# Kernel optimization log

Measured on AMD Instinct MI355X. Metric: run time of the kernel, lower is better.

## Reference

```python
import jax, jax.numpy as jnp
import numpy as np

B, L, D, H = 2, 2048, 1024, 16
DK = D // H  # 64


def setup_inputs() -> dict:
    key = jax.random.key(0)
    ks = jax.random.split(key, 9)
    s = 0.02
    return {
        "x": jax.random.normal(ks[0], (B, L, D), dtype=jnp.float32),
        "wq": jax.random.normal(ks[1], (D, D), dtype=jnp.float32) * s,
        "bq": jax.random.normal(ks[2], (D,), dtype=jnp.float32) * s,
        "wk": jax.random.normal(ks[3], (D, D), dtype=jnp.float32) * s,
        "bk": jax.random.normal(ks[4], (D,), dtype=jnp.float32) * s,
        "wv": jax.random.normal(ks[5], (D, D), dtype=jnp.float32) * s,
        "bv": jax.random.normal(ks[6], (D,), dtype=jnp.float32) * s,
        "wo": jax.random.normal(ks[7], (D, D), dtype=jnp.float32) * s,
        "bo": jax.random.normal(ks[8], (D,), dtype=jnp.float32) * s,
    }


def reference(x, wq, bq, wk, bk, wv, bv, wo, bo):
    b, l, d = x.shape
    # torch nn.Linear: y = x @ W^T + b
    q = (x @ wq.T + bq).reshape(b, l, H, DK).transpose(0, 2, 1, 3)  # (b,h,l,dk)
    k = (x @ wk.T + bk).reshape(b, l, H, DK).transpose(0, 2, 1, 3)
    v = (x @ wv.T + bv).reshape(b, l, H, DK).transpose(0, 2, 1, 3)
    scale = 1.0 / jnp.sqrt(jnp.asarray(DK, dtype=x.dtype))
    scores = jnp.einsum("bhqd,bhkd->bhqk", q, k) * scale  # (b,h,l,l)
    causal = jnp.triu(jnp.ones((l, l), dtype=bool), k=1)  # True above diagonal -> masked
    scores = jnp.where(causal[None, None], -jnp.inf, scores)
    probs = jax.nn.softmax(scores, axis=-1)
    out = jnp.einsum("bhqk,bhkd->bhqd", probs, v)  # (b,h,l,dk)
    out = out.transpose(0, 2, 1, 3).reshape(b, l, d)
    return out @ wo.T + bo
```

## Files before the change

### kernel.cpp

```cpp
#include <hip/hip_runtime.h>
#include <cstdint>

#define SEQ     2048
#define DMODEL  1024
#define NHEAD   16
#define DKH     64
#define NTOK    4096
#define LDQKV   3072

typedef __bf16 bf16x8 __attribute__((ext_vector_type(8)));
typedef __bf16 bf16x4 __attribute__((ext_vector_type(4)));
typedef float  f32x4  __attribute__((ext_vector_type(4)));

#define MFMA_BF16(a, b, c) __builtin_amdgcn_mfma_f32_16x16x32_bf16((a), (b), (c), 0, 0, 0)

#define C2F 0.18033688f

__device__ inline float fast_exp2(float x) {
#if __has_builtin(__builtin_amdgcn_exp2f)
  return __builtin_amdgcn_exp2f(x);
#else
  return __expf(x * 0.69314718056f);
#endif
}

__device__ inline void async_copy16(const void* g, void* l) {
  __builtin_amdgcn_global_load_lds(
      reinterpret_cast<const __attribute__((address_space(1))) void*>(
          reinterpret_cast<uintptr_t>(g)),
      reinterpret_cast<__attribute__((address_space(3))) void*>(
          reinterpret_cast<uintptr_t>(l)),
      16, 0, 0);
}

__device__ inline bf16x4 cvt4(float4 v) {
  bf16x4 r;
  r[0] = (__bf16)v.x; r[1] = (__bf16)v.y; r[2] = (__bf16)v.z; r[3] = (__bf16)v.w;
  return r;
}

__global__ __launch_bounds__(256) void pack_kernel(
    const float4* __restrict__ x,
    const float4* __restrict__ wq, const float4* __restrict__ wk,
    const float4* __restrict__ wv, const float4* __restrict__ wo,
    const float4* __restrict__ bq, const float4* __restrict__ bk,
    const float4* __restrict__ bv,
    bf16x4* __restrict__ xb, bf16x4* __restrict__ wqkv,
    bf16x4* __restrict__ wob, float4* __restrict__ bcat)
{
  const int NX = NTOK * DMODEL / 4;
  const int NW = DMODEL * DMODEL / 4;
  const int TOT = NX + 4 * NW + 3 * (DMODEL / 4);
  for (int g = blockIdx.x * 256 + threadIdx.x; g < TOT; g += gridDim.x * 256) {
    if (g < NX) {
      xb[g] = cvt4(x[g]);
    } else if (g < NX + 3 * NW) {
      int g2 = g - NX;
      const float4* s = (g2 < NW) ? wq : (g2 < 2 * NW ? wk : wv);
      float4 v = s[g2 & (NW - 1)];
      if (g2 < NW) { v.x *= C2F; v.y *= C2F; v.z *= C2F; v.w *= C2F; }
      wqkv[g2] = cvt4(v);
    } else if (g < NX + 4 * NW) {
      int g3 = g - NX - 3 * NW;
      wob[g3] = cvt4(wo[g3]);
    } else {
      int g4 = g - NX - 4 * NW;
      const float4* s = (g4 < 256) ? bq : (g4 < 512 ? bk : bv);
      float4 v = s[g4 & 255];
      if (g4 < 256) { v.x *= C2F; v.y *= C2F; v.z *= C2F; v.w *= C2F; }
      bcat[g4] = v;
    }
  }
}

template<int BN>
__global__ __launch_bounds__(256) void gemm_bias(
    const __bf16* __restrict__ A, const __bf16* __restrict__ W,
    const float* __restrict__ bias, void* __restrict__ C,
    int ldc, int out_bf16)
{
  constexpr int K = 1024;
  constexpr int JT = BN / 32;
  __shared__ __bf16 sA[2][128 * 32];
  __shared__ __bf16 sB[2][BN * 32];
  const int tid  = threadIdx.x;
  const int wave = tid >> 6, lane = tid & 63;
  const int quad = lane >> 4, l16 = lane & 15;
  const size_t m0 = (size_t)blockIdx.x * 128;
  const size_t n0 = (size_t)blockIdx.y * BN;
  const int wm = (wave & 1) * 64, wn = (wave >> 1) * (BN / 2);

  const int g0 = wave * 2;
  const int sr = lane >> 2;
  const int sc = (lane & 3) * 8;
  const __bf16* pa0 = A + (m0 + g0 * 16 + sr) * K + sc;
  const __bf16* pa1 = pa0 + 16 * K;
  const int brow = (BN == 128) ? g0 * 16 : wave * 16;
  const __bf16* pb0 = W + (n0 + brow + sr) * K + sc;
  const int lo  = g0 * 512;
  const int lob = (BN == 128) ? g0 * 512 : wave * 512;

  f32x4 acc[4][JT];
  const f32x4 z = {0.f, 0.f, 0.f, 0.f};
#pragma unroll
  for (int i = 0; i < 4; ++i)
#pragma unroll
    for (int j = 0; j < JT; ++j) acc[i][j] = z;

  async_copy16(pa0, &sA[0][lo]);
  async_copy16(pa1, &sA[0][lo + 512]);
  async_copy16(pb0, &sB[0][lob]);
  if (BN == 128) async_copy16(pb0 + 16 * K, &sB[0][lob + 512]);

  for (int k0 = 0; k0 < K; k0 += 32) {
    const int cur = (k0 >> 5) & 1, nxt = cur ^ 1;
    __syncthreads();
    if (k0 + 32 < K) {
      async_copy16(pa0 + k0 + 32, &sA[nxt][lo]);
      async_copy16(pa1 + k0 + 32, &sA[nxt][lo + 512]);
      async_copy16(pb0 + k0 + 32, &sB[nxt][lob]);
      if (BN == 128) async_copy16(pb0 + 16 * K + k0 + 32, &sB[nxt][lob + 512]);
    }

    bf16x8 af[4], bw[JT];
#pragma unroll
    for (int i = 0; i < 4; ++i)
      af[i] = *(const bf16x8*)(&sA[cur][(wm + i * 16 + l16) * 32 + quad * 8]);
#pragma unroll
    for (int j = 0; j < JT; ++j)
      bw[j] = *(const bf16x8*)(&sB[cur][(wn + j * 16 + l16) * 32 + quad * 8]);
#pragma unroll
    for (int i = 0; i < 4; ++i)
#pragma unroll
      for (int j = 0; j < JT; ++j)
        acc[i][j] = MFMA_BF16(af[i], bw[j], acc[i][j]);
  }

  float bi[JT];
#pragma unroll
  for (int j = 0; j < JT; ++j) bi[j] = bias[n0 + wn + j * 16 + l16];

#pragma unroll
  for (int i = 0; i < 4; ++i) {
#pragma unroll
    for (int j = 0; j < JT; ++j) {
#pragma unroll
      for (int r = 0; r < 4; ++r) {
        size_t row = m0 + wm + i * 16 + quad * 4 + r;
        size_t col = n0 + wn + j * 16 + l16;
        float v = acc[i][j][r] + bi[j];
        if (out_bf16) ((__bf16*)C)[row * ldc + col] = (__bf16)v;
        else          ((float*)C)[row * ldc + col] = v;
      }
    }
  }
}

__global__ __launch_bounds__(256) void vtrans_kernel(
    const __bf16* __restrict__ qkv, __bf16* __restrict__ vt)
{
  __shared__ __bf16 t[64][66];
  const int tid = threadIdx.x;
  const int bh = blockIdx.x;
  const int b = bh >> 4, h = bh & 15;
  const int l0 = blockIdx.y * 64;
  const int r4 = tid >> 6;
  const int c  = tid & 63;
#pragma unroll
  for (int rep = 0; rep < 16; ++rep) {
    int ll = rep * 4 + r4;
    t[ll][c] = qkv[(size_t)(b * SEQ + l0 + ll) * LDQKV + 2048 + h * DKH + c];
  }
  __syncthreads();
#pragma unroll
  for (int rep = 0; rep < 16; ++rep) {
    int dk = rep * 4 + r4;
    vt[(size_t)(bh * DKH + dk) * SEQ + l0 + c] = t[c][dk];
  }
}

__global__ __launch_bounds__(256) void attn_kernel(
    const __bf16* __restrict__ qkv,
    const __bf16* __restrict__ vt,
    __bf16* __restrict__ attn)
{
  __shared__ __bf16 sK[2][64 * 64];
  __shared__ __bf16 sV[2][64 * 64];
  __shared__ __bf16 pbuf[4][16 * 64];
  const int tid  = threadIdx.x;
  const int wave = tid >> 6, lane = tid & 63;
  const int quad = lane >> 4, l16 = lane & 15;
  const int id = blockIdx.x;
  const int u = (id >> 3) & 31, v = id & 7, w = id >> 8;
  const int bh = v * 4 + w;
  const int ue = u ^ ((w >> 1) << 3);
  const int qb = (w & 1) ? ue : 31 - ue;
  const int b = bh >> 4, h = bh & 15;
  const int q0 = qb * 64;
  const int qw = q0 + wave * 16;
  const size_t tokbase = (size_t)b * SEQ;

  const int srow = lane >> 3;
  const int sgr  = (lane & 7) ^ srow;
  const __bf16* pKsrc = qkv + (tokbase + wave * 16 + srow) * LDQKV + 1024 + h * DKH + sgr * 8;
  const __bf16* pVsrc = vt + ((size_t)bh * DKH + wave * 16 + srow) * SEQ + sgr * 8;
  const int lo = wave * 16 * 64;

  bf16x8 qf[2];
#pragma unroll
  for (int s = 0; s < 2; ++s)
    qf[s] = *(const bf16x8*)(qkv + (tokbase + qw + l16) * LDQKV + h * DKH + s * 32 + quad * 8);

  bf16x8 ones;
#pragma unroll
  for (int i = 0; i < 8; ++i) ones[i] = (__bf16)1.0f;

  f32x4 o[4], lacc;
  const f32x4 z = {0.f, 0.f, 0.f, 0.f};
#pragma unroll
  for (int t = 0; t < 4; ++t) o[t] = z;
  lacc = z;

  __bf16* pb = &pbuf[wave][0];
  const int swl = l16 & 7;

  async_copy16(pKsrc, &sK[0][lo]);
  async_copy16(pKsrc + (size_t)8 * LDQKV, &sK[0][lo + 8 * 64]);
  async_copy16(pVsrc, &sV[0][lo]);
  async_copy16(pVsrc + (size_t)8 * SEQ, &sV[0][lo + 8 * 64]);

  for (int t0 = 0; t0 <= qb; ++t0) {
    const int cur = t0 & 1, nxt = cur ^ 1;
    __syncthreads();
    if (t0 < qb) {
      const size_t koff = (size_t)(t0 + 1) * 64;
      async_copy16(pKsrc + koff * LDQKV, &sK[nxt][lo]);
      async_copy16(pKsrc + (koff + 8) * LDQKV, &sK[nxt][lo + 8 * 64]);
      async_copy16(pVsrc + koff, &sV[nxt][lo]);
      async_copy16(pVsrc + (size_t)8 * SEQ + koff, &sV[nxt][lo + 8 * 64]);
    }
    const __bf16* K_ = &sK[cur][0];
    const __bf16* V_ = &sV[cur][0];

    f32x4 sacc[4];
#pragma unroll
    for (int ct = 0; ct < 4; ++ct) {
      bf16x8 k0 = *(const bf16x8*)(K_ + (ct * 16 + l16) * 64 + ((quad ^ swl) * 8));
      bf16x8 k1 = *(const bf16x8*)(K_ + (ct * 16 + l16) * 64 + (((4 + quad) ^ swl) * 8));
      sacc[ct] = MFMA_BF16(k0, qf[0], z);
      sacc[ct] = MFMA_BF16(k1, qf[1], sacc[ct]);
    }

#pragma unroll
    for (int ct = 0; ct < 4; ++ct) {
      bf16x4 p4;
      if (t0 < qb) {
#pragma unroll
        for (int r = 0; r < 4; ++r) p4[r] = (__bf16)fast_exp2(sacc[ct][r]);
      } else {
#pragma unroll
        for (int r = 0; r < 4; ++r) {
          float sv = (ct * 16 + quad * 4 + r <= wave * 16 + l16) ? sacc[ct][r] : -1e30f;
          p4[r] = (__bf16)fast_exp2(sv);
        }
      }
      *(bf16x4*)(pb + l16 * 64 + (((ct * 4 + quad) ^ (swl << 1)) * 4)) = p4;
    }
    bf16x8 ap0 = *(const bf16x8*)(pb + l16 * 64 + ((quad ^ swl) * 8));
    bf16x8 ap1 = *(const bf16x8*)(pb + l16 * 64 + (((4 + quad) ^ swl) * 8));

    lacc = MFMA_BF16(ap0, ones, lacc);
    lacc = MFMA_BF16(ap1, ones, lacc);

#pragma unroll
    for (int dt = 0; dt < 4; ++dt) {
      bf16x8 v0 = *(const bf16x8*)(V_ + (dt * 16 + l16) * 64 + ((quad ^ swl) * 8));
      bf16x8 v1 = *(const bf16x8*)(V_ + (dt * 16 + l16) * 64 + (((4 + quad) ^ swl) * 8));
      o[dt] = MFMA_BF16(ap0, v0, o[dt]);
      o[dt] = MFMA_BF16(ap1, v1, o[dt]);
    }
  }

  float linv[4];
#pragma unroll
  for (int r = 0; r < 4; ++r) linv[r] = 1.0f / lacc[r];

#pragma unroll
  for (int dt = 0; dt < 4; ++dt)
#pragma unroll
    for (int r = 0; r < 4; ++r)
      attn[(tokbase + qw + quad * 4 + r) * DMODEL + h * DKH + dt * 16 + l16] =
          (__bf16)(o[dt][r] * linv[r]);
}

extern "C" void kernel_launch(void* const* d_in, const int* in_sizes, int n_in,
                              void* d_out, int out_size, void* d_ws, size_t ws_size,
                              hipStream_t stream) {
  const float* x  = (const float*)d_in[0];
  const float* wq = (const float*)d_in[1];
  const float* bq = (const float*)d_in[2];
  const float* wk = (const float*)d_in[3];
  const float* bk = (const float*)d_in[4];
  const float* wv = (const float*)d_in[5];
  const float* bv = (const float*)d_in[6];
  const float* wo = (const float*)d_in[7];
  const float* bo = (const float*)d_in[8];

  char* ws = (char*)d_ws;
  __bf16* xb    = (__bf16*)(ws + 0);
  __bf16* wqkv  = (__bf16*)(ws + 8388608);
  __bf16* wob   = (__bf16*)(ws + 14680064);
  float*  bcat  = (float*)(ws + 16777216);
  __bf16* qkv   = (__bf16*)(ws + 16789504);
  __bf16* vt    = (__bf16*)(ws + 41955328);
  __bf16* attn  = (__bf16*)(ws + 50343936);
  float*  out   = (float*)d_out;

  pack_kernel<<<1024, 256, 0, stream>>>(
      (const float4*)x, (const float4*)wq, (const float4*)wk, (const float4*)wv,
      (const float4*)wo, (const float4*)bq, (const float4*)bk, (const float4*)bv,
      (bf16x4*)xb, (bf16x4*)wqkv, (bf16x4*)wob, (float4*)bcat);

  gemm_bias<128><<<dim3(32, 24), 256, 0, stream>>>(xb, wqkv, bcat, qkv, LDQKV, 1);

  vtrans_kernel<<<dim3(32, 32), 256, 0, stream>>>(qkv, vt);

  attn_kernel<<<1024, 256, 0, stream>>>(qkv, vt, attn);

  gemm_bias<64><<<dim3(32, 16), 256, 0, stream>>>(attn, wob, bo, out, DMODEL, 0);
}
```

Baseline: 178.0 us.

## Process two 16-row query groups per wave in attention with 2-wave blocks

The attention kernel drops from four waves per block to two, and each wave now handles 32 query rows as two 16-row groups. Every K and V fragment read from shared memory is reused for both groups, which halves LDS reads per MFMA and doubles each thread's share of the async tile loads. In exchange, the per-wave register footprint grows (two sets of accumulators, scores and P fragments), and fewer threads per block may reduce latency hiding or occupancy.

```diff
diff --git a/kernel.cpp b/kernel.cpp
--- a/kernel.cpp
+++ b/kernel.cpp
@@ -179,14 +179,14 @@
   }
 }
 
-__global__ __launch_bounds__(256) void attn_kernel(
+__global__ __launch_bounds__(128) void attn_kernel(
     const __bf16* __restrict__ qkv,
     const __bf16* __restrict__ vt,
     __bf16* __restrict__ attn)
 {
   __shared__ __bf16 sK[2][64 * 64];
   __shared__ __bf16 sV[2][64 * 64];
-  __shared__ __bf16 pbuf[4][16 * 64];
+  __shared__ __bf16 pbuf[2][2][16 * 64];
   const int tid  = threadIdx.x;
   const int wave = tid >> 6, lane = tid & 63;
   const int quad = lane >> 4, l16 = lane & 15;
@@ -197,100 +197,126 @@
   const int qb = (w & 1) ? ue : 31 - ue;
   const int b = bh >> 4, h = bh & 15;
   const int q0 = qb * 64;
-  const int qw = q0 + wave * 16;
+  const int qw = q0 + wave * 32;
   const size_t tokbase = (size_t)b * SEQ;
 
   const int srow = lane >> 3;
   const int sgr  = (lane & 7) ^ srow;
-  const __bf16* pKsrc = qkv + (tokbase + wave * 16 + srow) * LDQKV + 1024 + h * DKH + sgr * 8;
-  const __bf16* pVsrc = vt + ((size_t)bh * DKH + wave * 16 + srow) * SEQ + sgr * 8;
-  const int lo = wave * 16 * 64;
-
-  bf16x8 qf[2];
-#pragma unroll
-  for (int s = 0; s < 2; ++s)
-    qf[s] = *(const bf16x8*)(qkv + (tokbase + qw + l16) * LDQKV + h * DKH + s * 32 + quad * 8);
+  const __bf16* pKsrc = qkv + (tokbase + wave * 32 + srow) * LDQKV + 1024 + h * DKH + sgr * 8;
+  const __bf16* pVsrc = vt + ((size_t)bh * DKH + wave * 32 + srow) * SEQ + sgr * 8;
+  const int lo = wave * 2048;
+
+  bf16x8 qf[2][2];
+#pragma unroll
+  for (int g = 0; g < 2; ++g)
+#pragma unroll
+    for (int s = 0; s < 2; ++s)
+      qf[g][s] = *(const bf16x8*)(qkv + (tokbase + qw + g * 16 + l16) * LDQKV + h * DKH + s * 32 + quad * 8);
 
   bf16x8 ones;
 #pragma unroll
   for (int i = 0; i < 8; ++i) ones[i] = (__bf16)1.0f;
 
-  f32x4 o[4], lacc;
+  f32x4 o[2][4], lacc[2];
   const f32x4 z = {0.f, 0.f, 0.f, 0.f};
 #pragma unroll
-  for (int t = 0; t < 4; ++t) o[t] = z;
-  lacc = z;
-
-  __bf16* pb = &pbuf[wave][0];
+  for (int g = 0; g < 2; ++g) {
+#pragma unroll
+    for (int t = 0; t < 4; ++t) o[g][t] = z;
+    lacc[g] = z;
+  }
+
+  __bf16* pbg[2] = { &pbuf[wave][0][0], &pbuf[wave][1][0] };
   const int swl = l16 & 7;
 
-  async_copy16(pKsrc, &sK[0][lo]);
-  async_copy16(pKsrc + (size_t)8 * LDQKV, &sK[0][lo + 8 * 64]);
-  async_copy16(pVsrc, &sV[0][lo]);
-  async_copy16(pVsrc + (size_t)8 * SEQ, &sV[0][lo + 8 * 64]);
+#pragma unroll
+  for (int k = 0; k < 4; ++k) {
+    async_copy16(pKsrc + (size_t)(8 * k) * LDQKV, &sK[0][lo + k * 512]);
+    async_copy16(pVsrc + (size_t)(8 * k) * SEQ,  &sV[0][lo + k * 512]);
+  }
 
   for (int t0 = 0; t0 <= qb; ++t0) {
     const int cur = t0 & 1, nxt = cur ^ 1;
     __syncthreads();
     if (t0 < qb) {
       const size_t koff = (size_t)(t0 + 1) * 64;
-      async_copy16(pKsrc + koff * LDQKV, &sK[nxt][lo]);
-      async_copy16(pKsrc + (koff + 8) * LDQKV, &sK[nxt][lo + 8 * 64]);
-      async_copy16(pVsrc + koff, &sV[nxt][lo]);
-      async_copy16(pVsrc + (size_t)8 * SEQ + koff, &sV[nxt][lo + 8 * 64]);
+#pragma unroll
+      for (int k = 0; k < 4; ++k) {
+        async_copy16(pKsrc + (koff + 8 * k) * LDQKV, &sK[nxt][lo + k * 512]);
+        async_copy16(pVsrc + koff + (size_t)(8 * k) * SEQ, &sV[nxt][lo + k * 512]);
+      }
     }
     const __bf16* K_ = &sK[cur][0];
     const __bf16* V_ = &sV[cur][0];
 
-    f32x4 sacc[4];
+    f32x4 sacc[2][4];
 #pragma unroll
     for (int ct = 0; ct < 4; ++ct) {
       bf16x8 k0 = *(const bf16x8*)(K_ + (ct * 16 + l16) * 64 + ((quad ^ swl) * 8));
       bf16x8 k1 = *(const bf16x8*)(K_ + (ct * 16 + l16) * 64 + (((4 + quad) ^ swl) * 8));
-      sacc[ct] = MFMA_BF16(k0, qf[0], z);
-      sacc[ct] = MFMA_BF16(k1, qf[1], sacc[ct]);
-    }
-
-#pragma unroll
-    for (int ct = 0; ct < 4; ++ct) {
-      bf16x4 p4;
-      if (t0 < qb) {
-#pragma unroll
-        for (int r = 0; r < 4; ++r) p4[r] = (__bf16)fast_exp2(sacc[ct][r]);
-      } else {
-#pragma unroll
-        for (int r = 0; r < 4; ++r) {
-          float sv = (ct * 16 + quad * 4 + r <= wave * 16 + l16) ? sacc[ct][r] : -1e30f;
-          p4[r] = (__bf16)fast_exp2(sv);
+      sacc[0][ct] = MFMA_BF16(k0, qf[0][0], z);
+      sacc[0][ct] = MFMA_BF16(k1, qf[0][1], sacc[0][ct]);
+      sacc[1][ct] = MFMA_BF16(k0, qf[1][0], z);
+      sacc[1][ct] = MFMA_BF16(k1, qf[1][1], sacc[1][ct]);
+    }
+
+#pragma unroll
+    for (int g = 0; g < 2; ++g) {
+      __bf16* pb = pbg[g];
+      const int off = 32 * wave + 16 * g;
+#pragma unroll
+      for (int ct = 0; ct < 4; ++ct) {
+        bf16x4 p4;
+        if (t0 < qb) {
+#pragma unroll
+          for (int r = 0; r < 4; ++r) p4[r] = (__bf16)fast_exp2(sacc[g][ct][r]);
+        } else {
+#pragma unroll
+          for (int r = 0; r < 4; ++r) {
+            float sv = (ct * 16 + quad * 4 + r <= off + l16) ? sacc[g][ct][r] : -1e30f;
+            p4[r] = (__bf16)fast_exp2(sv);
+          }
         }
+        *(bf16x4*)(pb + l16 * 64 + (((ct * 4 + quad) ^ (swl << 1)) * 4)) = p4;
       }
-      *(bf16x4*)(pb + l16 * 64 + (((ct * 4 + quad) ^ (swl << 1)) * 4)) = p4;
-    }
-    bf16x8 ap0 = *(const bf16x8*)(pb + l16 * 64 + ((quad ^ swl) * 8));
-    bf16x8 ap1 = *(const bf16x8*)(pb + l16 * 64 + (((4 + quad) ^ swl) * 8));
-
-    lacc = MFMA_BF16(ap0, ones, lacc);
-    lacc = MFMA_BF16(ap1, ones, lacc);
+    }
+
+    bf16x8 ap[2][2];
+#pragma unroll
+    for (int g = 0; g < 2; ++g) {
+      ap[g][0] = *(const bf16x8*)(pbg[g] + l16 * 64 + ((quad ^ swl) * 8));
+      ap[g][1] = *(const bf16x8*)(pbg[g] + l16 * 64 + (((4 + quad) ^ swl) * 8));
+    }
+
+#pragma unroll
+    for (int g = 0; g < 2; ++g) {
+      lacc[g] = MFMA_BF16(ap[g][0], ones, lacc[g]);
+      lacc[g] = MFMA_BF16(ap[g][1], ones, lacc[g]);
+    }
 
 #pragma unroll
     for (int dt = 0; dt < 4; ++dt) {
       bf16x8 v0 = *(const bf16x8*)(V_ + (dt * 16 + l16) * 64 + ((quad ^ swl) * 8));
       bf16x8 v1 = *(const bf16x8*)(V_ + (dt * 16 + l16) * 64 + (((4 + quad) ^ swl) * 8));
-      o[dt] = MFMA_BF16(ap0, v0, o[dt]);
-      o[dt] = MFMA_BF16(ap1, v1, o[dt]);
-    }
-  }
-
-  float linv[4];
-#pragma unroll
-  for (int r = 0; r < 4; ++r) linv[r] = 1.0f / lacc[r];
-
-#pragma unroll
-  for (int dt = 0; dt < 4; ++dt)
-#pragma unroll
-    for (int r = 0; r < 4; ++r)
-      attn[(tokbase + qw + quad * 4 + r) * DMODEL + h * DKH + dt * 16 + l16] =
-          (__bf16)(o[dt][r] * linv[r]);
+      o[0][dt] = MFMA_BF16(ap[0][0], v0, o[0][dt]);
+      o[0][dt] = MFMA_BF16(ap[0][1], v1, o[0][dt]);
+      o[1][dt] = MFMA_BF16(ap[1][0], v0, o[1][dt]);
+      o[1][dt] = MFMA_BF16(ap[1][1], v1, o[1][dt]);
+    }
+  }
+
+#pragma unroll
+  for (int g = 0; g < 2; ++g) {
+    float linv[4];
+#pragma unroll
+    for (int r = 0; r < 4; ++r) linv[r] = 1.0f / lacc[g][r];
+#pragma unroll
+    for (int dt = 0; dt < 4; ++dt)
+#pragma unroll
+      for (int r = 0; r < 4; ++r)
+        attn[(tokbase + qw + g * 16 + quad * 4 + r) * DMODEL + h * DKH + dt * 16 + l16] =
+            (__bf16)(o[g][dt][r] * linv[r]);
+  }
 }
 
 extern "C" void kernel_launch(void* const* d_in, const int* in_sizes, int n_in,
@@ -325,7 +351,7 @@
 
   vtrans_kernel<<<dim3(32, 32), 256, 0, stream>>>(qkv, vt);
 
-  attn_kernel<<<1024, 256, 0, stream>>>(qkv, vt, attn);
+  attn_kernel<<<1024, 128, 0, stream>>>(qkv, vt, attn);
 
   gemm_bias<64><<<dim3(32, 16), 256, 0, stream>>>(attn, wob, bo, out, DMODEL, 0);
 }
```

After: 188.3 us. 5.8% more time.

## Load K and V fragments directly from global memory instead of LDS double-buffering

Applied to the files above, without the earlier changes.

Removes the shared-memory double-buffered K/V tiles, their async copies and the per-iteration block barrier. Each wave now reads its K and V MFMA operands straight from global memory, relying on L1/L2 caching. s_setprio is also raised around the MFMA sections. This drops the barriers and LDS traffic, but each of the four waves now reloads the same K/V data from global memory and the loads are no longer prefetched one tile ahead, so load latency sits directly on the critical path.

```diff
diff --git a/kernel.cpp b/kernel.cpp
--- a/kernel.cpp
+++ b/kernel.cpp
@@ -184,8 +184,6 @@
     const __bf16* __restrict__ vt,
     __bf16* __restrict__ attn)
 {
-  __shared__ __bf16 sK[2][64 * 64];
-  __shared__ __bf16 sV[2][64 * 64];
   __shared__ __bf16 pbuf[4][16 * 64];
   const int tid  = threadIdx.x;
   const int wave = tid >> 6, lane = tid & 63;
@@ -200,12 +198,6 @@
   const int qw = q0 + wave * 16;
   const size_t tokbase = (size_t)b * SEQ;
 
-  const int srow = lane >> 3;
-  const int sgr  = (lane & 7) ^ srow;
-  const __bf16* pKsrc = qkv + (tokbase + wave * 16 + srow) * LDQKV + 1024 + h * DKH + sgr * 8;
-  const __bf16* pVsrc = vt + ((size_t)bh * DKH + wave * 16 + srow) * SEQ + sgr * 8;
-  const int lo = wave * 16 * 64;
-
   bf16x8 qf[2];
 #pragma unroll
   for (int s = 0; s < 2; ++s)
@@ -224,32 +216,23 @@
   __bf16* pb = &pbuf[wave][0];
   const int swl = l16 & 7;
 
-  async_copy16(pKsrc, &sK[0][lo]);
-  async_copy16(pKsrc + (size_t)8 * LDQKV, &sK[0][lo + 8 * 64]);
-  async_copy16(pVsrc, &sV[0][lo]);
-  async_copy16(pVsrc + (size_t)8 * SEQ, &sV[0][lo + 8 * 64]);
+  const __bf16* Kl = qkv + (tokbase + l16) * LDQKV + 1024 + h * DKH + quad * 8;
+  const __bf16* Vl = vt + ((size_t)bh * DKH + l16) * SEQ + quad * 8;
 
   for (int t0 = 0; t0 <= qb; ++t0) {
-    const int cur = t0 & 1, nxt = cur ^ 1;
-    __syncthreads();
-    if (t0 < qb) {
-      const size_t koff = (size_t)(t0 + 1) * 64;
-      async_copy16(pKsrc + koff * LDQKV, &sK[nxt][lo]);
-      async_copy16(pKsrc + (koff + 8) * LDQKV, &sK[nxt][lo + 8 * 64]);
-      async_copy16(pVsrc + koff, &sV[nxt][lo]);
-      async_copy16(pVsrc + (size_t)8 * SEQ + koff, &sV[nxt][lo + 8 * 64]);
-    }
-    const __bf16* K_ = &sK[cur][0];
-    const __bf16* V_ = &sV[cur][0];
+    const __bf16* Kt = Kl + (size_t)t0 * 64 * LDQKV;
+    const __bf16* Vt = Vl + t0 * 64;
 
     f32x4 sacc[4];
+    __builtin_amdgcn_s_setprio(1);
 #pragma unroll
     for (int ct = 0; ct < 4; ++ct) {
-      bf16x8 k0 = *(const bf16x8*)(K_ + (ct * 16 + l16) * 64 + ((quad ^ swl) * 8));
-      bf16x8 k1 = *(const bf16x8*)(K_ + (ct * 16 + l16) * 64 + (((4 + quad) ^ swl) * 8));
+      bf16x8 k0 = *(const bf16x8*)(Kt + (size_t)(ct * 16) * LDQKV);
+      bf16x8 k1 = *(const bf16x8*)(Kt + (size_t)(ct * 16) * LDQKV + 32);
       sacc[ct] = MFMA_BF16(k0, qf[0], z);
       sacc[ct] = MFMA_BF16(k1, qf[1], sacc[ct]);
     }
+    __builtin_amdgcn_s_setprio(0);
 
 #pragma unroll
     for (int ct = 0; ct < 4; ++ct) {
@@ -269,16 +252,18 @@
     bf16x8 ap0 = *(const bf16x8*)(pb + l16 * 64 + ((quad ^ swl) * 8));
     bf16x8 ap1 = *(const bf16x8*)(pb + l16 * 64 + (((4 + quad) ^ swl) * 8));
 
+    __builtin_amdgcn_s_setprio(1);
     lacc = MFMA_BF16(ap0, ones, lacc);
     lacc = MFMA_BF16(ap1, ones, lacc);
 
 #pragma unroll
     for (int dt = 0; dt < 4; ++dt) {
-      bf16x8 v0 = *(const bf16x8*)(V_ + (dt * 16 + l16) * 64 + ((quad ^ swl) * 8));
-      bf16x8 v1 = *(const bf16x8*)(V_ + (dt * 16 + l16) * 64 + (((4 + quad) ^ swl) * 8));
+      bf16x8 v0 = *(const bf16x8*)(Vt + (size_t)(dt * 16) * SEQ);
+      bf16x8 v1 = *(const bf16x8*)(Vt + (size_t)(dt * 16) * SEQ + 32);
       o[dt] = MFMA_BF16(ap0, v0, o[dt]);
       o[dt] = MFMA_BF16(ap1, v1, o[dt]);
     }
+    __builtin_amdgcn_s_setprio(0);
   }
 
   float linv[4];
```

New measurement: 264.7 us. +48.7%, slower.

## Split long causal query blocks across two workgroups and combine partial outputs

Applied to the files above, without the earlier changes.

Query blocks 16-31, which have the most causal key tiles, are split into two halves along the key dimension. Each half is processed by its own workgroup, which writes unnormalized fp32 partial outputs and row sums. A new combine kernel adds the halves and normalizes them. The goal is to balance load and shorten the tail of the attention kernel, at the cost of an extra launch and extra fp32 partial traffic. It also drops the previous block-order swizzle.

```diff
diff --git a/kernel.cpp b/kernel.cpp
--- a/kernel.cpp
+++ b/kernel.cpp
@@ -182,7 +182,9 @@
 __global__ __launch_bounds__(256) void attn_kernel(
     const __bf16* __restrict__ qkv,
     const __bf16* __restrict__ vt,
-    __bf16* __restrict__ attn)
+    __bf16* __restrict__ attn,
+    float* __restrict__ Opart,
+    float* __restrict__ lpart)
 {
   __shared__ __bf16 sK[2][64 * 64];
   __shared__ __bf16 sV[2][64 * 64];
@@ -191,13 +193,22 @@
   const int wave = tid >> 6, lane = tid & 63;
   const int quad = lane >> 4, l16 = lane & 15;
   const int id = blockIdx.x;
-  const int u = (id >> 3) & 31, v = id & 7, w = id >> 8;
-  const int bh = v * 4 + w;
-  const int ue = u ^ ((w >> 1) << 3);
-  const int qb = (w & 1) ? ue : 31 - ue;
+  const int bh = id & 31;
+  const int u  = id >> 5;
+  int qb, t_lo, t_hi, rec;
+  if (u < 32) {
+    qb = 31 - (u >> 1);
+    const int nh = (qb + 1) >> 1;
+    const int half = u & 1;
+    t_lo = half ? nh : 0;
+    t_hi = half ? qb + 1 : nh;
+    rec  = (bh * 16 + (qb - 16)) * 2 + half;
+  } else {
+    qb = 47 - u;
+    t_lo = 0; t_hi = qb + 1; rec = -1;
+  }
   const int b = bh >> 4, h = bh & 15;
-  const int q0 = qb * 64;
-  const int qw = q0 + wave * 16;
+  const int qw = qb * 64 + wave * 16;
   const size_t tokbase = (size_t)b * SEQ;
 
   const int srow = lane >> 3;
@@ -224,15 +235,19 @@
   __bf16* pb = &pbuf[wave][0];
   const int swl = l16 & 7;
 
-  async_copy16(pKsrc, &sK[0][lo]);
-  async_copy16(pKsrc + (size_t)8 * LDQKV, &sK[0][lo + 8 * 64]);
-  async_copy16(pVsrc, &sV[0][lo]);
-  async_copy16(pVsrc + (size_t)8 * SEQ, &sV[0][lo + 8 * 64]);
-
-  for (int t0 = 0; t0 <= qb; ++t0) {
+  {
+    const size_t koff = (size_t)t_lo * 64;
+    const int b0 = t_lo & 1;
+    async_copy16(pKsrc + koff * LDQKV, &sK[b0][lo]);
+    async_copy16(pKsrc + (koff + 8) * LDQKV, &sK[b0][lo + 8 * 64]);
+    async_copy16(pVsrc + koff, &sV[b0][lo]);
+    async_copy16(pVsrc + (size_t)8 * SEQ + koff, &sV[b0][lo + 8 * 64]);
+  }
+
+  for (int t0 = t_lo; t0 < t_hi; ++t0) {
     const int cur = t0 & 1, nxt = cur ^ 1;
     __syncthreads();
-    if (t0 < qb) {
+    if (t0 + 1 < t_hi) {
       const size_t koff = (size_t)(t0 + 1) * 64;
       async_copy16(pKsrc + koff * LDQKV, &sK[nxt][lo]);
       async_copy16(pKsrc + (koff + 8) * LDQKV, &sK[nxt][lo + 8 * 64]);
@@ -281,16 +296,58 @@
     }
   }
 
-  float linv[4];
-#pragma unroll
-  for (int r = 0; r < 4; ++r) linv[r] = 1.0f / lacc[r];
-
-#pragma unroll
-  for (int dt = 0; dt < 4; ++dt)
-#pragma unroll
-    for (int r = 0; r < 4; ++r)
-      attn[(tokbase + qw + quad * 4 + r) * DMODEL + h * DKH + dt * 16 + l16] =
-          (__bf16)(o[dt][r] * linv[r]);
+  if (rec < 0) {
+    float linv[4];
+#pragma unroll
+    for (int r = 0; r < 4; ++r) linv[r] = 1.0f / lacc[r];
+#pragma unroll
+    for (int dt = 0; dt < 4; ++dt)
+#pragma unroll
+      for (int r = 0; r < 4; ++r)
+        attn[(tokbase + qw + quad * 4 + r) * DMODEL + h * DKH + dt * 16 + l16] =
+            (__bf16)(o[dt][r] * linv[r]);
+  } else {
+    float* Op = Opart + (size_t)rec * 4096;
+#pragma unroll
+    for (int dt = 0; dt < 4; ++dt)
+#pragma unroll
+      for (int r = 0; r < 4; ++r)
+        Op[(wave * 16 + quad * 4 + r) * 64 + dt * 16 + l16] = o[dt][r];
+    if (l16 == 0) {
+#pragma unroll
+      for (int r = 0; r < 4; ++r)
+        lpart[rec * 64 + wave * 16 + quad * 4 + r] = lacc[r];
+    }
+  }
+}
+
+__global__ __launch_bounds__(256) void combine_kernel(
+    const float* __restrict__ Opart, const float* __restrict__ lpart,
+    __bf16* __restrict__ attn)
+{
+  const int blk = blockIdx.x;
+  const int bh = blk >> 4, qs = 16 + (blk & 15);
+  const int b = bh >> 4, h = bh & 15;
+  const int tid = threadIdx.x;
+  const int q  = tid >> 2;
+  const int d0 = (tid & 3) * 16;
+  const int recA = blk * 2, recB = recA + 1;
+  const float lsum = lpart[recA * 64 + q] + lpart[recB * 64 + q];
+  const float linv = 1.0f / lsum;
+  const float4* OA = (const float4*)(Opart + (size_t)recA * 4096 + q * 64 + d0);
+  const float4* OB = (const float4*)(Opart + (size_t)recB * 4096 + q * 64 + d0);
+  const size_t tok = (size_t)b * SEQ + qs * 64 + q;
+  __bf16* dst = attn + tok * DMODEL + h * DKH + d0;
+#pragma unroll
+  for (int j = 0; j < 4; ++j) {
+    float4 a = OA[j], c = OB[j];
+    bf16x4 o4;
+    o4[0] = (__bf16)((a.x + c.x) * linv);
+    o4[1] = (__bf16)((a.y + c.y) * linv);
+    o4[2] = (__bf16)((a.z + c.z) * linv);
+    o4[3] = (__bf16)((a.w + c.w) * linv);
+    *(bf16x4*)(dst + j * 4) = o4;
+  }
 }
 
 extern "C" void kernel_launch(void* const* d_in, const int* in_sizes, int n_in,
@@ -314,6 +371,8 @@
   __bf16* qkv   = (__bf16*)(ws + 16789504);
   __bf16* vt    = (__bf16*)(ws + 41955328);
   __bf16* attn  = (__bf16*)(ws + 50343936);
+  float*  Opart = (float*)(ws + 67108864);
+  float*  lpart = (float*)(ws + 83886080);
   float*  out   = (float*)d_out;
 
   pack_kernel<<<1024, 256, 0, stream>>>(
@@ -325,7 +384,9 @@
 
   vtrans_kernel<<<dim3(32, 32), 256, 0, stream>>>(qkv, vt);
 
-  attn_kernel<<<1024, 256, 0, stream>>>(qkv, vt, attn);
+  attn_kernel<<<1536, 256, 0, stream>>>(qkv, vt, attn, Opart, lpart);
+
+  combine_kernel<<<512, 256, 0, stream>>>(Opart, lpart, attn);
 
   gemm_bias<64><<<dim3(32, 16), 256, 0, stream>>>(attn, wob, bo, out, DMODEL, 0);
 }
```

Measured after the change: 187.0 us. 1.05x slower.
